# Kernel optimization log

Hardware: AMD Instinct MI355X
Metric: run time of the kernel (lower is better)

## Reference

```python
import jax, jax.numpy as jnp
import numpy as np

# ---- sedenion multiplication table via Cayley-Dickson construction ----
def _cd_conj(x):
    if x.shape[0] == 1:
        return x
    h = x.shape[0] // 2
    return np.concatenate([_cd_conj(x[:h]), -x[h:]])

def _cd_mult(x, y):
    n = x.shape[0]
    if n == 1:
        return x * y
    h = n // 2
    a, b = x[:h], x[h:]
    c, d = y[:h], y[h:]
    return np.concatenate([
        _cd_mult(a, c) - _cd_mult(_cd_conj(d), b),
        _cd_mult(d, a) + _cd_mult(b, _cd_conj(c)),
    ])

def _sed_table():
    T = np.zeros((16, 16, 16), dtype=np.float32)
    I = np.eye(16, dtype=np.float32)
    for i in range(16):
        for j in range(16):
            r = _cd_mult(I[i], I[j])  # e_i * e_j = sign * e_k
            k = int(np.abs(r).argmax())
            T[i, j, k] = r[k]
    return T

_T = jnp.asarray(_sed_table())  # [16,16,16] constant sign table

DIM = 128
MLP_RATIO = 4
EPS = 1e-5

def _ln(x, g, b):
    m = jnp.mean(x, axis=-1, keepdims=True)
    v = jnp.mean((x - m) ** 2, axis=-1, keepdims=True)
    return (x - m) * jax.lax.rsqrt(v + EPS) * g + b

def setup_inputs() -> dict:
    key = jax.random.key(0)
    ks = jax.random.split(key, 8)
    C, Ch = DIM, DIM * MLP_RATIO
    s = 1.0 / np.sqrt(C)
    inp = {
        "x": jax.random.normal(ks[0], (8, C, 128, 128), dtype=jnp.float32),
        "gamma1": jnp.ones((C,), jnp.float32),
        "beta1": jnp.zeros((C,), jnp.float32),
        "sed_w": jax.random.normal(ks[1], (16, C, C), jnp.float32) * (s / 4.0),
        "w_proj": jax.random.normal(ks[2], (C, C), jnp.float32) * s,
        "b_proj": jnp.zeros((C,), jnp.float32),
        "gamma2": jnp.ones((C,), jnp.float32),
        "beta2": jnp.zeros((C,), jnp.float32),
        "w1": jax.random.normal(ks[3], (C, Ch), jnp.float32) * s,
        "b1": jnp.zeros((Ch,), jnp.float32),
        "w2": jax.random.normal(ks[4], (Ch, C), jnp.float32) * (1.0 / np.sqrt(Ch)),
        "b2": jnp.zeros((C,), jnp.float32),
    }
    return inp

def reference(x, gamma1, beta1, sed_w, w_proj, b_proj, gamma2, beta2, w1, b1, w2, b2):
    B, C, H, W = x.shape  # H, W divisible by 4 -> no padding branch
    h, w = H // 4, W // 4
    xt = jnp.transpose(x, (0, 2, 3, 1))          # [B,H,W,C]
    # norm1
    xn = _ln(xt, gamma1, beta1)
    # window partition: 'b c (h s1)(w s2) -> b h w (s1 s2 c)'
    xw = xn.reshape(B, h, 4, w, 4, C).transpose(0, 1, 3, 2, 4, 5).reshape(B, h, w, 16, C)
    # SedenionLinear: y_k = sum_{i,j} T[i,j,k] * x_i @ W_j  (bias=False)
    ys = jnp.einsum('bhwic,ijk,jcd->bhwkd', xw, _T, sed_w)
    # reverse window + to bhwc
    y = ys.reshape(B, h, w, 4, 4, C).transpose(0, 1, 3, 2, 4, 5).reshape(B, H, W, C)
    # act + proj
    y = jax.nn.gelu(y, approximate=False)
    y = y @ w_proj + b_proj
    # residual 1
    y = xt + y
    # norm2 + MLP + residual 2
    m = _ln(y, gamma2, beta2)
    m = jax.nn.gelu(m @ w1 + b1, approximate=False)
    m = m @ w2 + b2
    out = y + m
    return jnp.transpose(out, (0, 3, 1, 2))  # back to [B,C,H,W]
```

## Files before the change

### kernel.cpp

```cpp
#include <hip/hip_runtime.h>
#include <hip/hip_bf16.h>

#define DEVI __device__ __forceinline__

typedef __attribute__((ext_vector_type(8))) __bf16 bf16x8;
typedef __attribute__((ext_vector_type(4))) __bf16 bf16x4;
typedef __attribute__((ext_vector_type(4))) float f32x4;

using bf16 = __hip_bfloat16;

DEVI float bf2f(bf16 v) { return __bfloat162float(v); }
DEVI bf16 f2bf(float v) { return __float2bfloat16(v); }

DEVI float gelu_fast(float v) {
    float t = v * (2.30220777f + 0.10294322f * v * v);
    float e = __builtin_amdgcn_exp2f(t);
    return v - v * __builtin_amdgcn_rcpf(e + 1.0f);
}

DEVI void async16(void* lds, const void* g) {
    __builtin_amdgcn_global_load_lds(
        (const __attribute__((address_space(1))) void*)g,
        (__attribute__((address_space(3))) void*)lds, 16, 0, 0);
}

DEVI int cd_sign(int i, int j) {
    int s = 1, n = 16;
    while (n > 1) {
        int h = n >> 1;
        int ih = (i >= h), jh = (j >= h);
        if (!ih && !jh) {
        } else if (!ih && jh) {
            int ni = j - h, nj = i;
            i = ni; j = nj;
        } else if (ih && !jh) {
            if (j != 0) s = -s;
            i = i - h;
        } else {
            int ni = j - h, nj = i - h;
            if (ni == 0) s = -s;
            i = ni; j = nj;
        }
        n = h;
    }
    return s;
}

__global__ __launch_bounds__(256) void k_prep_A(const float* __restrict__ sed_w,
                                                bf16* __restrict__ At) {
    __shared__ float tile[128][129];
    int bi = blockIdx.x;
    int i = bi >> 4, k = bi & 15;
    int j = i ^ k;
    float s = (float)cd_sign(i, j);
    int t = threadIdx.x;
    int lo = t & 127, hi = t >> 7;
    const float* src = sed_w + j * 16384;
    for (int it = 0; it < 64; ++it) {
        int c = it * 2 + hi;
        tile[c][lo] = src[c * 128 + lo];
    }
    __syncthreads();
    for (int it = 0; it < 64; ++it) {
        int d = it * 2 + hi;
        At[(long)(k * 128 + d) * 2048 + i * 128 + lo] = f2bf(s * tile[lo][d]);
    }
}

__global__ __launch_bounds__(256) void k_prep_w(const float* __restrict__ wp,
                                                const float* __restrict__ w1,
                                                const float* __restrict__ w2,
                                                bf16* __restrict__ wpT,
                                                bf16* __restrict__ w1T,
                                                bf16* __restrict__ w2T) {
    int idx = blockIdx.x * 256 + threadIdx.x;
    if (idx < 16384) {
        int d = idx >> 7, c = idx & 127;
        wpT[idx] = f2bf(wp[c * 128 + d]);
    } else if (idx < 16384 + 65536) {
        int e = idx - 16384;
        int o = e >> 7, c = e & 127;
        w1T[e] = f2bf(w1[c * 512 + o]);
    } else if (idx < 16384 + 131072) {
        int e = idx - 81920;
        int o = e >> 9, c = e & 511;
        w2T[e] = f2bf(w2[c * 128 + o]);
    }
}

__global__ __launch_bounds__(256) void k_ln1(const float* __restrict__ x,
                                             const float* __restrict__ g,
                                             const float* __restrict__ bta,
                                             bf16* __restrict__ xt,
                                             bf16* __restrict__ xn) {
    __shared__ float tile[128][128];
    __shared__ float ps[2][128], pss[2][128];
    int b = blockIdx.x >> 7, r = blockIdx.x & 127;
    int t = threadIdx.x, c = t & 127, half = t >> 7;
    const float* xb = x + ((long)b * 128 * 128 + r) * 128;
    for (int it = 0; it < 64; ++it) {
        int ch = it * 2 + half;
        tile[ch][c] = xb[(long)ch * 16384 + c];
    }
    __syncthreads();
    float s = 0.f, ss = 0.f;
    for (int ch = half * 64; ch < half * 64 + 64; ++ch) {
        float v = tile[ch][c];
        s += v; ss += v * v;
    }
    ps[half][c] = s; pss[half][c] = ss;
    __syncthreads();
    float S = ps[0][c] + ps[1][c], SS = pss[0][c] + pss[1][c];
    float mean = S * (1.f / 128.f);
    float var = SS * (1.f / 128.f) - mean * mean;
    float rstd = rsqrtf(var + 1e-5f);
    long n = (((long)b * 32 + (r >> 2)) * 32 + (c >> 2)) * 16 + ((r & 3) * 4 + (c & 3));
    bf16* xtr = xt + n * 128 + half * 64;
    bf16* xnr = xn + n * 128 + half * 64;
#pragma unroll
    for (int v8 = 0; v8 < 8; ++v8) {
        bf16x8 pt, pn;
#pragma unroll
        for (int e = 0; e < 8; ++e) {
            int ch = half * 64 + v8 * 8 + e;
            float v = tile[ch][c];
            pt[e] = (__bf16)v;
            pn[e] = (__bf16)((v - mean) * rstd * g[ch] + bta[ch]);
        }
        *(bf16x8*)&xtr[v8 * 8] = pt;
        *(bf16x8*)&xnr[v8 * 8] = pn;
    }
}

__global__ __launch_bounds__(512, 2) void k_gemm_sed(const bf16* __restrict__ At,
                                                     const bf16* __restrict__ xn,
                                                     bf16* __restrict__ g_) {
    extern __shared__ __align__(16) char buf[];
    const int t = threadIdx.x;
    const long bn = (long)blockIdx.x * 256;
    const long bm = (long)blockIdx.y * 256;
    const int lane = t & 63;
    const int wid = t >> 6;
    const int wm2 = wid >> 2;
    const int wn4 = wid & 3;
    const int l15 = lane & 15, quad = lane >> 4;

    const int srow = t >> 3;
    const int sslot = (t & 7) ^ (srow & 7);
    const bf16* gA0 = At + (bm + srow) * 2048L + sslot * 8;
    const bf16* gB0 = xn + (bn + srow) * 2048L + sslot * 8;

    char* const ldsA = buf;
    char* const ldsB = buf + 65536;

    const int ax0 = ((quad + 0) ^ (l15 & 7)) << 4;
    const int ax1 = ((quad + 4) ^ (l15 & 7)) << 4;
    const int aRowBase = wm2 * 16384 + l15 * 128;
    const int bRowBase = (wn4 >> 1) * 16384 + ((wn4 & 1) * 64 + l15) * 128;

#define SED_STAGE(d, kt)                                                     \
    {                                                                        \
        const long k0_ = (long)(kt) * 64;                                    \
        char* la_ = ldsA + (d) * 32768;                                      \
        char* lb_ = ldsB + (d) * 32768;                                      \
        const bf16* ga_ = gA0 + k0_;                                         \
        const bf16* gb_ = gB0 + k0_;                                         \
        _Pragma("unroll")                                                    \
        for (int h_ = 0; h_ < 2; ++h_)                                       \
            _Pragma("unroll")                                                \
            for (int r_ = 0; r_ < 2; ++r_) {                                 \
                const long gro_ = (long)(h_ * 128 + r_ * 64) * 2048;         \
                const int lo_ = h_ * 16384 + r_ * 8192 + t * 16;             \
                async16(la_ + lo_, ga_ + gro_);                              \
                async16(lb_ + lo_, gb_ + gro_);                              \
            }                                                                \
    }

    SED_STAGE(0, 0);
    SED_STAGE(1, 1);

    f32x4 acc[8][4] = {};

    for (int tt = 0; tt < 32; ++tt) {
        const int d = tt & 1;
        if (tt < 31) asm volatile("s_waitcnt vmcnt(8)" ::: "memory");
        else         asm volatile("s_waitcnt vmcnt(0)" ::: "memory");
        __builtin_amdgcn_s_barrier();
        asm volatile("" ::: "memory");

        char* const la = ldsA + d * 32768 + aRowBase;
        char* const lb = ldsB + d * 32768 + bRowBase;
#pragma unroll
        for (int p = 0; p < 4; ++p) {
            const int kk = p & 1, mh = p >> 1;
            const int xo = kk ? ax1 : ax0;
            bf16x8 af[4], bfr[4];
#pragma unroll
            for (int i = 0; i < 4; ++i)
                af[i] = *(const bf16x8*)(la + (mh * 4 + i) * 2048 + xo);
#pragma unroll
            for (int n = 0; n < 4; ++n)
                bfr[n] = *(const bf16x8*)(lb + n * 2048 + xo);
            __builtin_amdgcn_s_barrier();
            __builtin_amdgcn_s_setprio(1);
#pragma unroll
            for (int i = 0; i < 4; ++i)
#pragma unroll
                for (int n = 0; n < 4; ++n)
                    acc[mh * 4 + i][n] = __builtin_amdgcn_mfma_f32_16x16x32_bf16(
                        af[i], bfr[n], acc[mh * 4 + i][n], 0, 0, 0);
            __builtin_amdgcn_s_setprio(0);
            __builtin_amdgcn_s_barrier();
        }
        if (tt < 30) {
            asm volatile("" ::: "memory");
            SED_STAGE(d, tt + 2);
        }
    }
#undef SED_STAGE

    __syncthreads();
    bf16* sOut = (bf16*)buf;
#pragma unroll
    for (int p2 = 0; p2 < 2; ++p2) {
        if (wm2 == p2) {
#pragma unroll
            for (int m = 0; m < 8; ++m)
#pragma unroll
                for (int n = 0; n < 4; ++n) {
                    int win = wn4 * 64 + n * 16 + l15;
                    int kdl = m * 16 + quad * 4;
                    bf16x4 v;
#pragma unroll
                    for (int r = 0; r < 4; ++r)
                        v[r] = (__bf16)gelu_fast(acc[m][n][r]);
                    int slot = kdl >> 3;
                    int off = win * 256 + ((slot ^ (win & 7)) << 4) +
                              ((kdl * 2) & 15);
                    *(bf16x4*)((char*)sOut + off) = v;
                }
        }
        __syncthreads();
#pragma unroll
        for (int rr = 0; rr < 2; ++rr) {
            int win = (t >> 2) + rr * 128;
            int sub = t & 3;
#pragma unroll
            for (int j = 0; j < 4; ++j) {
                int c = j * 4 + sub;
                bf16x8 v = *(const bf16x8*)((char*)sOut + win * 256 +
                                            ((c ^ (win & 7)) << 4));
                *(bf16x8*)&g_[(bn + win) * 2048L + bm + p2 * 128 + c * 8] = v;
            }
        }
        __syncthreads();
    }
}

__global__ __launch_bounds__(256, 2) void k_tail(
    const bf16* __restrict__ g_,
    const bf16* __restrict__ wpT,
    const float* __restrict__ bproj,
    const bf16* __restrict__ xt,
    const float* __restrict__ gamma2, const float* __restrict__ beta2,
    const bf16* __restrict__ w1T,
    const float* __restrict__ b1,
    const bf16* __restrict__ w2T,
    const float* __restrict__ b2,
    float* __restrict__ out)
{
    __shared__ __align__(16) char buf[71680];
    bf16* mpT = (bf16*)buf;
    float* stats = (float*)(buf + 34816);
    float* outF = (float*)buf;

    int t = threadIdx.x;
    long tb = (long)blockIdx.x * 128;
    int lane = t & 63;
    int wm = ((t >> 7) & 1) * 64;
    int wm1 = ((t >> 7) & 1) * 32;
    int wn = ((t >> 6) & 1) * 64;
    int l15 = lane & 15, quad = lane >> 4;
    int half = wm >> 6;

    int tok[4];
#pragma unroll
    for (int tn = 0; tn < 4; ++tn) tok[tn] = wn + tn * 16 + l15;

    f32x4 acc1[4][4] = {};
#pragma unroll
    for (int k0 = 0; k0 < 128; k0 += 32) {
        bf16x8 af[4], bfr[4];
#pragma unroll
        for (int tm = 0; tm < 4; ++tm)
            af[tm] = *(const bf16x8*)&wpT[(wm + tm * 16 + l15) * 128 + k0 + quad * 8];
#pragma unroll
        for (int tn = 0; tn < 4; ++tn)
            bfr[tn] = *(const bf16x8*)&g_[(tb + tok[tn]) * 128 + k0 + quad * 8];
#pragma unroll
        for (int tm = 0; tm < 4; ++tm)
#pragma unroll
            for (int tn = 0; tn < 4; ++tn)
                acc1[tm][tn] = __builtin_amdgcn_mfma_f32_16x16x32_bf16(
                    af[tm], bfr[tn], acc1[tm][tn], 0, 0, 0);
    }

#pragma unroll
    for (int tm = 0; tm < 4; ++tm) {
        int c0 = wm + tm * 16 + quad * 4;
        float4 bp = *(const float4*)&bproj[c0];
#pragma unroll
        for (int tn = 0; tn < 4; ++tn) {
            bf16x4 xv = *(const bf16x4*)&xt[(tb + tok[tn]) * 128 + c0];
#pragma unroll
            for (int reg = 0; reg < 4; ++reg)
                acc1[tm][tn][reg] += ((const float*)&bp)[reg] + (float)xv[reg];
        }
    }

#pragma unroll
    for (int tn = 0; tn < 4; ++tn) {
        float s = 0.f, ss = 0.f;
#pragma unroll
        for (int tm = 0; tm < 4; ++tm)
#pragma unroll
            for (int reg = 0; reg < 4; ++reg) {
                float v = acc1[tm][tn][reg];
                s += v; ss += v * v;
            }
        s += __shfl_xor(s, 16); ss += __shfl_xor(ss, 16);
        s += __shfl_xor(s, 32); ss += __shfl_xor(ss, 32);
        if (quad == 0) {
            stats[tok[tn] * 2 + half] = s;
            stats[256 + tok[tn] * 2 + half] = ss;
        }
    }
    __syncthreads();

    float mean[4], rstd[4];
#pragma unroll
    for (int tn = 0; tn < 4; ++tn) {
        float S = stats[tok[tn] * 2] + stats[tok[tn] * 2 + 1];
        float SS = stats[256 + tok[tn] * 2] + stats[256 + tok[tn] * 2 + 1];
        mean[tn] = S * (1.f / 128.f);
        float var = SS * (1.f / 128.f) - mean[tn] * mean[tn];
        rstd[tn] = rsqrtf(var + 1e-5f);
    }
#pragma unroll
    for (int tm = 0; tm < 4; ++tm) {
        int c0 = wm + tm * 16 + quad * 4;
        float4 gv = *(const float4*)&gamma2[c0];
        float4 bv = *(const float4*)&beta2[c0];
#pragma unroll
        for (int tn = 0; tn < 4; ++tn) {
            bf16x4 p;
#pragma unroll
            for (int reg = 0; reg < 4; ++reg)
                p[reg] = (__bf16)((acc1[tm][tn][reg] - mean[tn]) * rstd[tn] *
                                      ((const float*)&gv)[reg] +
                                  ((const float*)&bv)[reg]);
            *(bf16x4*)&mpT[tok[tn] * 136 + c0] = p;
        }
    }
    __syncthreads();

    f32x4 acc2[4][4] = {};
    for (int oh = 0; oh < 8; ++oh) {
        bf16* hT = (bf16*)(buf + 34816 + (oh & 1) * 18432);
        f32x4 acch[2][4] = {};
#pragma unroll
        for (int k0 = 0; k0 < 128; k0 += 32) {
            bf16x8 af[2], bfr[4];
#pragma unroll
            for (int tm = 0; tm < 2; ++tm)
                af[tm] = *(const bf16x8*)&w1T[(oh * 64 + wm1 + tm * 16 + l15) * 128 +
                                              k0 + quad * 8];
#pragma unroll
            for (int tn = 0; tn < 4; ++tn)
                bfr[tn] = *(const bf16x8*)&mpT[tok[tn] * 136 + k0 + quad * 8];
#pragma unroll
            for (int tm = 0; tm < 2; ++tm)
#pragma unroll
                for (int tn = 0; tn < 4; ++tn)
                    acch[tm][tn] = __builtin_amdgcn_mfma_f32_16x16x32_bf16(
                        af[tm], bfr[tn], acch[tm][tn], 0, 0, 0);
        }
#pragma unroll
        for (int tm = 0; tm < 2; ++tm) {
            int hc0 = wm1 + tm * 16 + quad * 4;
            float4 bh = *(const float4*)&b1[oh * 64 + hc0];
#pragma unroll
            for (int tn = 0; tn < 4; ++tn) {
                bf16x4 p;
#pragma unroll
                for (int reg = 0; reg < 4; ++reg)
                    p[reg] = (__bf16)gelu_fast(acch[tm][tn][reg] +
                                               ((const float*)&bh)[reg]);
                *(bf16x4*)&hT[tok[tn] * 72 + hc0] = p;
            }
        }
        __syncthreads();
#pragma unroll
        for (int k0 = 0; k0 < 64; k0 += 32) {
            bf16x8 af[4], bfr[4];
#pragma unroll
            for (int tm = 0; tm < 4; ++tm)
                af[tm] = *(const bf16x8*)&w2T[(wm + tm * 16 + l15) * 512 +
                                              oh * 64 + k0 + quad * 8];
#pragma unroll
            for (int tn = 0; tn < 4; ++tn)
                bfr[tn] = *(const bf16x8*)&hT[tok[tn] * 72 + k0 + quad * 8];
#pragma unroll
            for (int tm = 0; tm < 4; ++tm)
#pragma unroll
                for (int tn = 0; tn < 4; ++tn)
                    acc2[tm][tn] = __builtin_amdgcn_mfma_f32_16x16x32_bf16(
                        af[tm], bfr[tn], acc2[tm][tn], 0, 0, 0);
        }
    }
    __syncthreads();

    long win0 = tb >> 4;
    int b = (int)(win0 >> 10);
    int hq = (int)(win0 >> 5) & 31;
    int wq0 = (int)win0 & 31;
#pragma unroll
    for (int p = 0; p < 2; ++p) {
#pragma unroll
        for (int tmi = 0; tmi < 2; ++tmi) {
            int tm = p * 2 + tmi;
            int c0 = wm + tm * 16 + quad * 4;
            int slot0 = (wm >> 1) + tmi * 16 + quad * 4;
            float4 bv = *(const float4*)&b2[c0];
#pragma unroll
            for (int tn = 0; tn < 4; ++tn)
#pragma unroll
                for (int reg = 0; reg < 4; ++reg)
                    outF[(slot0 + reg) * 132 + tok[tn]] =
                        acc1[tm][tn][reg] + acc2[tm][tn][reg] +
                        ((const float*)&bv)[reg];
        }
        __syncthreads();
#pragma unroll
        for (int it = 0; it < 8; ++it) {
            int id = it * 256 + t;
            int slot = id >> 5, rem = id & 31;
            int rr = rem >> 3, wqo = rem & 7;
            int c = slot + ((slot >= 32) ? 32 : 0) + p * 32;
            f32x4 v = *(const f32x4*)&outF[slot * 132 + wqo * 16 + rr * 4];
            long addr = (((long)b * 128 + c) * 128 + hq * 4 + rr) * 128 +
                        (wq0 + wqo) * 4;
            *(f32x4*)&out[addr] = v;
        }
        __syncthreads();
    }
}

extern "C" void kernel_launch(void* const* d_in, const int* in_sizes, int n_in,
                              void* d_out, int out_size, void* d_ws, size_t ws_size,
                              hipStream_t stream) {
    const float* x      = (const float*)d_in[0];
    const float* gamma1 = (const float*)d_in[1];
    const float* beta1  = (const float*)d_in[2];
    const float* sed_w  = (const float*)d_in[3];
    const float* w_proj = (const float*)d_in[4];
    const float* b_proj = (const float*)d_in[5];
    const float* gamma2 = (const float*)d_in[6];
    const float* beta2  = (const float*)d_in[7];
    const float* w1     = (const float*)d_in[8];
    const float* b1     = (const float*)d_in[9];
    const float* w2     = (const float*)d_in[10];
    const float* b2     = (const float*)d_in[11];

    char* ws = (char*)d_ws;
    bf16* At  = (bf16*)(ws + 0);
    bf16* wpT = (bf16*)(ws + 8388608);
    bf16* w1T = (bf16*)(ws + 8421376);
    bf16* w2T = (bf16*)(ws + 8552448);
    bf16* xt  = (bf16*)(ws + 8683520);
    bf16* xn  = (bf16*)(ws + 42237952);
    bf16* g_  = (bf16*)(ws + 75792384);

    hipLaunchKernelGGL(k_prep_w, dim3(576), dim3(256), 0, stream,
                       w_proj, w1, w2, wpT, w1T, w2T);
    hipLaunchKernelGGL(k_prep_A, dim3(256), dim3(256), 0, stream, sed_w, At);
    hipLaunchKernelGGL(k_ln1, dim3(1024), dim3(256), 0, stream,
                       x, gamma1, beta1, xt, xn);
    hipLaunchKernelGGL(k_gemm_sed, dim3(32, 8), dim3(512), 131072, stream,
                       At, xn, g_);
    hipLaunchKernelGGL(k_tail, dim3(1024), dim3(256), 0, stream,
                       g_, wpT, b_proj, xt, gamma2, beta2,
                       w1T, b1, w2T, b2, (float*)d_out);
}
```

Before: 335.6 us.

## Assign each wave its own 32 tokens in tail kernel to drop block syncs

Reorganizes the tail kernel's warp tiling so each of the four waves owns 32 tokens across all 128 channels, instead of a 2x2 split over channels and tokens. LayerNorm statistics can then be reduced entirely within a wave, which removes the LDS stats exchange and its barriers. The per-iteration __syncthreads in the MLP loop also goes away because each wave reads only its own hidden tile, and LDS use shrinks. In exchange, every wave now loads all of the weight rows, which increases redundant global/L2 weight traffic, and the larger A-fragment arrays may raise register pressure.

```diff
diff --git a/kernel.cpp b/kernel.cpp
--- a/kernel.cpp
+++ b/kernel.cpp
@@ -269,60 +269,59 @@
     const float* __restrict__ b2,
     float* __restrict__ out)
 {
-    __shared__ __align__(16) char buf[71680];
+    __shared__ __align__(16) char buf[53248];
     bf16* mpT = (bf16*)buf;
-    float* stats = (float*)(buf + 34816);
+    bf16* hTb = (bf16*)(buf + 34816);
     float* outF = (float*)buf;
 
     int t = threadIdx.x;
     long tb = (long)blockIdx.x * 128;
     int lane = t & 63;
-    int wm = ((t >> 7) & 1) * 64;
-    int wm1 = ((t >> 7) & 1) * 32;
-    int wn = ((t >> 6) & 1) * 64;
+    int wid = t >> 6;
+    int twid = wid * 32;
     int l15 = lane & 15, quad = lane >> 4;
-    int half = wm >> 6;
-
-    int tok[4];
-#pragma unroll
-    for (int tn = 0; tn < 4; ++tn) tok[tn] = wn + tn * 16 + l15;
-
-    f32x4 acc1[4][4] = {};
+
+    bf16* mpW = mpT + twid * 136;
+    bf16* hW  = hTb + twid * 72;
+
+    f32x4 acc1[8][2] = {};
 #pragma unroll
     for (int k0 = 0; k0 < 128; k0 += 32) {
-        bf16x8 af[4], bfr[4];
-#pragma unroll
-        for (int tm = 0; tm < 4; ++tm)
-            af[tm] = *(const bf16x8*)&wpT[(wm + tm * 16 + l15) * 128 + k0 + quad * 8];
-#pragma unroll
-        for (int tn = 0; tn < 4; ++tn)
-            bfr[tn] = *(const bf16x8*)&g_[(tb + tok[tn]) * 128 + k0 + quad * 8];
-#pragma unroll
-        for (int tm = 0; tm < 4; ++tm)
-#pragma unroll
-            for (int tn = 0; tn < 4; ++tn)
+        bf16x8 af[8], bfr[2];
+#pragma unroll
+        for (int tm = 0; tm < 8; ++tm)
+            af[tm] = *(const bf16x8*)&wpT[(tm * 16 + l15) * 128 + k0 + quad * 8];
+#pragma unroll
+        for (int tn = 0; tn < 2; ++tn)
+            bfr[tn] = *(const bf16x8*)&g_[(tb + twid + tn * 16 + l15) * 128 +
+                                          k0 + quad * 8];
+#pragma unroll
+        for (int tm = 0; tm < 8; ++tm)
+#pragma unroll
+            for (int tn = 0; tn < 2; ++tn)
                 acc1[tm][tn] = __builtin_amdgcn_mfma_f32_16x16x32_bf16(
                     af[tm], bfr[tn], acc1[tm][tn], 0, 0, 0);
     }
 
 #pragma unroll
-    for (int tm = 0; tm < 4; ++tm) {
-        int c0 = wm + tm * 16 + quad * 4;
+    for (int tm = 0; tm < 8; ++tm) {
+        int c0 = tm * 16 + quad * 4;
         float4 bp = *(const float4*)&bproj[c0];
 #pragma unroll
-        for (int tn = 0; tn < 4; ++tn) {
-            bf16x4 xv = *(const bf16x4*)&xt[(tb + tok[tn]) * 128 + c0];
+        for (int tn = 0; tn < 2; ++tn) {
+            bf16x4 xv = *(const bf16x4*)&xt[(tb + twid + tn * 16 + l15) * 128 + c0];
 #pragma unroll
             for (int reg = 0; reg < 4; ++reg)
                 acc1[tm][tn][reg] += ((const float*)&bp)[reg] + (float)xv[reg];
         }
     }
 
-#pragma unroll
-    for (int tn = 0; tn < 4; ++tn) {
+    float mean[2], rstd[2];
+#pragma unroll
+    for (int tn = 0; tn < 2; ++tn) {
         float s = 0.f, ss = 0.f;
 #pragma unroll
-        for (int tm = 0; tm < 4; ++tm)
+        for (int tm = 0; tm < 8; ++tm)
 #pragma unroll
             for (int reg = 0; reg < 4; ++reg) {
                 float v = acc1[tm][tn][reg];
@@ -330,90 +329,84 @@
             }
         s += __shfl_xor(s, 16); ss += __shfl_xor(ss, 16);
         s += __shfl_xor(s, 32); ss += __shfl_xor(ss, 32);
-        if (quad == 0) {
-            stats[tok[tn] * 2 + half] = s;
-            stats[256 + tok[tn] * 2 + half] = ss;
-        }
-    }
-    __syncthreads();
-
-    float mean[4], rstd[4];
-#pragma unroll
-    for (int tn = 0; tn < 4; ++tn) {
-        float S = stats[tok[tn] * 2] + stats[tok[tn] * 2 + 1];
-        float SS = stats[256 + tok[tn] * 2] + stats[256 + tok[tn] * 2 + 1];
-        mean[tn] = S * (1.f / 128.f);
-        float var = SS * (1.f / 128.f) - mean[tn] * mean[tn];
+        mean[tn] = s * (1.f / 128.f);
+        float var = ss * (1.f / 128.f) - mean[tn] * mean[tn];
         rstd[tn] = rsqrtf(var + 1e-5f);
     }
-#pragma unroll
-    for (int tm = 0; tm < 4; ++tm) {
-        int c0 = wm + tm * 16 + quad * 4;
+
+#pragma unroll
+    for (int tm = 0; tm < 8; ++tm) {
+        int c0 = tm * 16 + quad * 4;
         float4 gv = *(const float4*)&gamma2[c0];
         float4 bv = *(const float4*)&beta2[c0];
 #pragma unroll
-        for (int tn = 0; tn < 4; ++tn) {
+        for (int tn = 0; tn < 2; ++tn) {
             bf16x4 p;
 #pragma unroll
             for (int reg = 0; reg < 4; ++reg)
                 p[reg] = (__bf16)((acc1[tm][tn][reg] - mean[tn]) * rstd[tn] *
                                       ((const float*)&gv)[reg] +
                                   ((const float*)&bv)[reg]);
-            *(bf16x4*)&mpT[tok[tn] * 136 + c0] = p;
-        }
-    }
-    __syncthreads();
-
-    f32x4 acc2[4][4] = {};
+            *(bf16x4*)&mpW[(tn * 16 + l15) * 136 + c0] = p;
+        }
+    }
+
+    f32x4 acc2[8][2];
+#pragma unroll
+    for (int tm = 0; tm < 8; ++tm)
+#pragma unroll
+        for (int tn = 0; tn < 2; ++tn)
+            acc2[tm][tn] = acc1[tm][tn];
+
     for (int oh = 0; oh < 8; ++oh) {
-        bf16* hT = (bf16*)(buf + 34816 + (oh & 1) * 18432);
-        f32x4 acch[2][4] = {};
+        f32x4 acch[4][2] = {};
 #pragma unroll
         for (int k0 = 0; k0 < 128; k0 += 32) {
-            bf16x8 af[2], bfr[4];
-#pragma unroll
-            for (int tm = 0; tm < 2; ++tm)
-                af[tm] = *(const bf16x8*)&w1T[(oh * 64 + wm1 + tm * 16 + l15) * 128 +
+            bf16x8 af[4], bfr[2];
+#pragma unroll
+            for (int tm = 0; tm < 4; ++tm)
+                af[tm] = *(const bf16x8*)&w1T[(oh * 64 + tm * 16 + l15) * 128 +
                                               k0 + quad * 8];
 #pragma unroll
-            for (int tn = 0; tn < 4; ++tn)
-                bfr[tn] = *(const bf16x8*)&mpT[tok[tn] * 136 + k0 + quad * 8];
-#pragma unroll
-            for (int tm = 0; tm < 2; ++tm)
-#pragma unroll
-                for (int tn = 0; tn < 4; ++tn)
+            for (int tn = 0; tn < 2; ++tn)
+                bfr[tn] = *(const bf16x8*)&mpW[(tn * 16 + l15) * 136 +
+                                               k0 + quad * 8];
+#pragma unroll
+            for (int tm = 0; tm < 4; ++tm)
+#pragma unroll
+                for (int tn = 0; tn < 2; ++tn)
                     acch[tm][tn] = __builtin_amdgcn_mfma_f32_16x16x32_bf16(
                         af[tm], bfr[tn], acch[tm][tn], 0, 0, 0);
         }
 #pragma unroll
-        for (int tm = 0; tm < 2; ++tm) {
-            int hc0 = wm1 + tm * 16 + quad * 4;
+        for (int tm = 0; tm < 4; ++tm) {
+            int hc0 = tm * 16 + quad * 4;
             float4 bh = *(const float4*)&b1[oh * 64 + hc0];
 #pragma unroll
-            for (int tn = 0; tn < 4; ++tn) {
+            for (int tn = 0; tn < 2; ++tn) {
                 bf16x4 p;
 #pragma unroll
                 for (int reg = 0; reg < 4; ++reg)
                     p[reg] = (__bf16)gelu_fast(acch[tm][tn][reg] +
                                                ((const float*)&bh)[reg]);
-                *(bf16x4*)&hT[tok[tn] * 72 + hc0] = p;
+                *(bf16x4*)&hW[(tn * 16 + l15) * 72 + hc0] = p;
             }
         }
-        __syncthreads();
 #pragma unroll
         for (int k0 = 0; k0 < 64; k0 += 32) {
-            bf16x8 af[4], bfr[4];
-#pragma unroll
-            for (int tm = 0; tm < 4; ++tm)
-                af[tm] = *(const bf16x8*)&w2T[(wm + tm * 16 + l15) * 512 +
+            bf16x8 af[8], bfr[2];
+#pragma unroll
+            for (int tm = 0; tm < 8; ++tm)
+                af[tm] = *(const bf16x8*)&w2T[(tm * 16 + l15) * 512 +
                                               oh * 64 + k0 + quad * 8];
 #pragma unroll
-            for (int tn = 0; tn < 4; ++tn)
-                bfr[tn] = *(const bf16x8*)&hT[tok[tn] * 72 + k0 + quad * 8];
-#pragma unroll
-            for (int tm = 0; tm < 4; ++tm)
-#pragma unroll
-                for (int tn = 0; tn < 4; ++tn)
+            for (int tn = 0; tn < 2; ++tn)
+                bfr[tn] = *(const bf16x8*)&hW[(tn * 16 + l15) * 72 +
+                                              k0 + quad * 8];
+#pragma unroll
+            for (int tm = 0; tm < 8; ++tm)
+#pragma unroll
+                for (int tn = 0; tn < 2; ++tn)
                     acc2[tm][tn] = __builtin_amdgcn_mfma_f32_16x16x32_bf16(
                         af[tm], bfr[tn], acc2[tm][tn], 0, 0, 0);
         }
@@ -427,18 +420,17 @@
 #pragma unroll
     for (int p = 0; p < 2; ++p) {
 #pragma unroll
-        for (int tmi = 0; tmi < 2; ++tmi) {
-            int tm = p * 2 + tmi;
-            int c0 = wm + tm * 16 + quad * 4;
-            int slot0 = (wm >> 1) + tmi * 16 + quad * 4;
+        for (int tmi = 0; tmi < 4; ++tmi) {
+            int tm = p * 4 + tmi;
+            int c0 = tm * 16 + quad * 4;
+            int slot0 = tmi * 16 + quad * 4;
             float4 bv = *(const float4*)&b2[c0];
 #pragma unroll
-            for (int tn = 0; tn < 4; ++tn)
+            for (int tn = 0; tn < 2; ++tn)
 #pragma unroll
                 for (int reg = 0; reg < 4; ++reg)
-                    outF[(slot0 + reg) * 132 + tok[tn]] =
-                        acc1[tm][tn][reg] + acc2[tm][tn][reg] +
-                        ((const float*)&bv)[reg];
+                    outF[(slot0 + reg) * 132 + twid + tn * 16 + l15] =
+                        acc2[tm][tn][reg] + ((const float*)&bv)[reg];
         }
         __syncthreads();
 #pragma unroll
@@ -446,7 +438,7 @@
             int id = it * 256 + t;
             int slot = id >> 5, rem = id & 31;
             int rr = rem >> 3, wqo = rem & 7;
-            int c = slot + ((slot >= 32) ? 32 : 0) + p * 32;
+            int c = p * 64 + slot;
             f32x4 v = *(const f32x4*)&outF[slot * 132 + wqo * 16 + rr * 4];
             long addr = (((long)b * 128 + c) * 128 + hq * 4 + rr) * 128 +
                         (wq0 + wqo) * 4;
```

Result: slower. 390.9 us (+16.5%).

## Split MLP hidden dim across wave pairs to remove per-chunk block barriers

Applied to the files above, without the earlier changes.

The MLP loop is restructured so each wave pair handles its own slice of hidden channels and computes all 128 output channels for its tokens. The GELU hidden tile goes into a per-wave private LDS region, which removes the block-wide __syncthreads inside the hidden loop and shrinks shared memory. The two halves' partial second-GEMM results are summed through LDS in the epilogue, with the residual folded into one half's accumulators. In exchange each wave keeps twice as many accumulators (8x4 f32x4), which raises register pressure and may force spills or lower occupancy under launch_bounds(256,2).

```diff
diff --git a/kernel.cpp b/kernel.cpp
--- a/kernel.cpp
+++ b/kernel.cpp
@@ -269,19 +269,22 @@
     const float* __restrict__ b2,
     float* __restrict__ out)
 {
-    __shared__ __align__(16) char buf[71680];
+    __shared__ __align__(16) char buf[55296];
     bf16* mpT = (bf16*)buf;
+    bf16* hTb = (bf16*)(buf + 34816);
     float* stats = (float*)(buf + 34816);
     float* outF = (float*)buf;
 
     int t = threadIdx.x;
     long tb = (long)blockIdx.x * 128;
     int lane = t & 63;
-    int wm = ((t >> 7) & 1) * 64;
-    int wm1 = ((t >> 7) & 1) * 32;
+    int wid = t >> 6;
+    int b = (t >> 7) & 1;
+    int wm = b * 64;
     int wn = ((t >> 6) & 1) * 64;
     int l15 = lane & 15, quad = lane >> 4;
-    int half = wm >> 6;
+
+    bf16* hW = hTb + wid * 64 * 40;
 
     int tok[4];
 #pragma unroll
@@ -331,8 +334,8 @@
         s += __shfl_xor(s, 16); ss += __shfl_xor(ss, 16);
         s += __shfl_xor(s, 32); ss += __shfl_xor(ss, 32);
         if (quad == 0) {
-            stats[tok[tn] * 2 + half] = s;
-            stats[256 + tok[tn] * 2 + half] = ss;
+            stats[tok[tn] * 2 + b] = s;
+            stats[256 + tok[tn] * 2 + b] = ss;
         }
     }
     __syncthreads();
@@ -364,16 +367,27 @@
     }
     __syncthreads();
 
-    f32x4 acc2[4][4] = {};
-    for (int oh = 0; oh < 8; ++oh) {
-        bf16* hT = (bf16*)(buf + 34816 + (oh & 1) * 18432);
+    f32x4 acc2[8][4];
+#pragma unroll
+    for (int tm = 0; tm < 8; ++tm)
+#pragma unroll
+        for (int tn = 0; tn < 4; ++tn)
+            acc2[tm][tn] = f32x4{0.f, 0.f, 0.f, 0.f};
+#pragma unroll
+    for (int tmi = 0; tmi < 4; ++tmi)
+#pragma unroll
+        for (int tn = 0; tn < 4; ++tn)
+            acc2[b * 4 + tmi][tn] = acc1[tmi][tn];
+
+    for (int c = 0; c < 8; ++c) {
+        int ohh = c * 2 + b;
         f32x4 acch[2][4] = {};
 #pragma unroll
         for (int k0 = 0; k0 < 128; k0 += 32) {
             bf16x8 af[2], bfr[4];
 #pragma unroll
             for (int tm = 0; tm < 2; ++tm)
-                af[tm] = *(const bf16x8*)&w1T[(oh * 64 + wm1 + tm * 16 + l15) * 128 +
+                af[tm] = *(const bf16x8*)&w1T[(ohh * 32 + tm * 16 + l15) * 128 +
                                               k0 + quad * 8];
 #pragma unroll
             for (int tn = 0; tn < 4; ++tn)
@@ -387,8 +401,8 @@
         }
 #pragma unroll
         for (int tm = 0; tm < 2; ++tm) {
-            int hc0 = wm1 + tm * 16 + quad * 4;
-            float4 bh = *(const float4*)&b1[oh * 64 + hc0];
+            int hc0 = tm * 16 + quad * 4;
+            float4 bh = *(const float4*)&b1[ohh * 32 + hc0];
 #pragma unroll
             for (int tn = 0; tn < 4; ++tn) {
                 bf16x4 p;
@@ -396,49 +410,60 @@
                 for (int reg = 0; reg < 4; ++reg)
                     p[reg] = (__bf16)gelu_fast(acch[tm][tn][reg] +
                                                ((const float*)&bh)[reg]);
-                *(bf16x4*)&hT[tok[tn] * 72 + hc0] = p;
+                *(bf16x4*)&hW[(tn * 16 + l15) * 40 + hc0] = p;
             }
         }
-        __syncthreads();
-#pragma unroll
-        for (int k0 = 0; k0 < 64; k0 += 32) {
-            bf16x8 af[4], bfr[4];
-#pragma unroll
-            for (int tm = 0; tm < 4; ++tm)
-                af[tm] = *(const bf16x8*)&w2T[(wm + tm * 16 + l15) * 512 +
-                                              oh * 64 + k0 + quad * 8];
+        bf16x8 af2[8], bfr2[4];
+#pragma unroll
+        for (int tm = 0; tm < 8; ++tm)
+            af2[tm] = *(const bf16x8*)&w2T[(tm * 16 + l15) * 512 +
+                                           ohh * 32 + quad * 8];
+#pragma unroll
+        for (int tn = 0; tn < 4; ++tn)
+            bfr2[tn] = *(const bf16x8*)&hW[(tn * 16 + l15) * 40 + quad * 8];
+#pragma unroll
+        for (int tm = 0; tm < 8; ++tm)
 #pragma unroll
             for (int tn = 0; tn < 4; ++tn)
-                bfr[tn] = *(const bf16x8*)&hT[tok[tn] * 72 + k0 + quad * 8];
-#pragma unroll
-            for (int tm = 0; tm < 4; ++tm)
-#pragma unroll
-                for (int tn = 0; tn < 4; ++tn)
-                    acc2[tm][tn] = __builtin_amdgcn_mfma_f32_16x16x32_bf16(
-                        af[tm], bfr[tn], acc2[tm][tn], 0, 0, 0);
-        }
+                acc2[tm][tn] = __builtin_amdgcn_mfma_f32_16x16x32_bf16(
+                    af2[tm], bfr2[tn], acc2[tm][tn], 0, 0, 0);
     }
     __syncthreads();
 
     long win0 = tb >> 4;
-    int b = (int)(win0 >> 10);
+    int bb = (int)(win0 >> 10);
     int hq = (int)(win0 >> 5) & 31;
     int wq0 = (int)win0 & 31;
 #pragma unroll
     for (int p = 0; p < 2; ++p) {
-#pragma unroll
-        for (int tmi = 0; tmi < 2; ++tmi) {
-            int tm = p * 2 + tmi;
-            int c0 = wm + tm * 16 + quad * 4;
-            int slot0 = (wm >> 1) + tmi * 16 + quad * 4;
-            float4 bv = *(const float4*)&b2[c0];
-#pragma unroll
-            for (int tn = 0; tn < 4; ++tn)
-#pragma unroll
-                for (int reg = 0; reg < 4; ++reg)
-                    outF[(slot0 + reg) * 132 + tok[tn]] =
-                        acc1[tm][tn][reg] + acc2[tm][tn][reg] +
-                        ((const float*)&bv)[reg];
+        if (b == 0) {
+#pragma unroll
+            for (int tmi = 0; tmi < 4; ++tmi) {
+                int tm = p * 4 + tmi;
+                int c0 = tm * 16 + quad * 4;
+                int slot0 = tmi * 16 + quad * 4;
+                float4 bv = *(const float4*)&b2[c0];
+#pragma unroll
+                for (int tn = 0; tn < 4; ++tn)
+#pragma unroll
+                    for (int reg = 0; reg < 4; ++reg)
+                        outF[(slot0 + reg) * 132 + tok[tn]] =
+                            acc2[tm][tn][reg] + ((const float*)&bv)[reg];
+            }
+        }
+        __syncthreads();
+        if (b == 1) {
+#pragma unroll
+            for (int tmi = 0; tmi < 4; ++tmi) {
+                int tm = p * 4 + tmi;
+                int slot0 = tmi * 16 + quad * 4;
+#pragma unroll
+                for (int tn = 0; tn < 4; ++tn)
+#pragma unroll
+                    for (int reg = 0; reg < 4; ++reg)
+                        outF[(slot0 + reg) * 132 + tok[tn]] +=
+                            acc2[tm][tn][reg];
+            }
         }
         __syncthreads();
 #pragma unroll
@@ -446,9 +471,9 @@
             int id = it * 256 + t;
             int slot = id >> 5, rem = id & 31;
             int rr = rem >> 3, wqo = rem & 7;
-            int c = slot + ((slot >= 32) ? 32 : 0) + p * 32;
+            int ch = p * 64 + slot;
             f32x4 v = *(const f32x4*)&outF[slot * 132 + wqo * 16 + rr * 4];
-            long addr = (((long)b * 128 + c) * 128 + hq * 4 + rr) * 128 +
+            long addr = (((long)bb * 128 + ch) * 128 + hq * 4 + rr) * 128 +
                         (wq0 + wqo) * 4;
             *(f32x4*)&out[addr] = v;
         }
```

After: 405.8 us. +20.9%, slower.
